# Kernel optimization log

Measured on AMD Instinct MI355X. Metric: run time of the kernel, lower is better.

## Reference

```python
import jax, jax.numpy as jnp
import numpy as np

DIM = 256
D_STATE = 16
D_INNER = 2 * DIM
D_CONV = 4
DT_RANK = (DIM + 15) // 16  # 'auto' = ceil(dim/16)
B_SZ, H, W = 8, 32, 32


def setup_inputs() -> dict:
    key = jax.random.key(0)
    ks = jax.random.split(key, 12)
    n = lambda k, s, sc=0.02: jax.random.normal(k, s, jnp.float32) * sc
    # Mamba1 dt init: dt ~ exp(U(log dt_min, log dt_max)), bias = inv_softplus(dt)
    dt = jnp.exp(jax.random.uniform(ks[5], (D_INNER,), jnp.float32,
                                    np.log(1e-3), np.log(1e-1)))
    return {
        "x": jax.random.normal(ks[0], (B_SZ, DIM, H, W), jnp.float32),
        "ln_g": jnp.ones((DIM,), jnp.float32),
        "ln_b": jnp.zeros((DIM,), jnp.float32),
        "in_proj_w": n(ks[1], (2 * D_INNER, DIM)),
        "conv_w": n(ks[2], (D_INNER, 1, D_CONV), 0.1),  # depthwise Conv1d kernel
        "conv_b": jnp.zeros((D_INNER,), jnp.float32),
        "x_proj_w": n(ks[3], (DT_RANK + 2 * D_STATE, D_INNER)),
        "dt_proj_w": n(ks[4], (D_INNER, DT_RANK), DT_RANK ** -0.5),
        "dt_proj_b": jnp.log(jnp.expm1(dt)),
        "A_log": jnp.log(jnp.broadcast_to(
            jnp.arange(1, D_STATE + 1, dtype=jnp.float32), (D_INNER, D_STATE))),
        "Dp": jnp.ones((D_INNER,), jnp.float32),
        "out_proj_w": n(ks[6], (DIM, D_INNER)),
        "mlp_ln_g": jnp.ones((DIM,), jnp.float32),
        "mlp_ln_b": jnp.zeros((DIM,), jnp.float32),
        "mlp_w1": n(ks[7], (4 * DIM, DIM)),
        "mlp_b1": jnp.zeros((4 * DIM,), jnp.float32),
        "mlp_w2": n(ks[8], (DIM, 4 * DIM)),
        "mlp_b2": jnp.zeros((DIM,), jnp.float32),
    }


def _layernorm(x, g, b):
    m = x.mean(-1, keepdims=True)
    v = x.var(-1, keepdims=True)
    return (x - m) * jax.lax.rsqrt(v + 1e-5) * g + b


def _selective_scan(u, dt, A, Bm, Cm, Dp):
    # u, dt: [B,L,Di]; Bm, Cm: [B,L,S]; A: [Di,S]; Dp: [Di]
    def step(h, t):
        dt_t, B_t, C_t, u_t = t  # [B,Di], [B,S], [B,S], [B,Di]
        dA = jnp.exp(dt_t[..., None] * A)                 # [B,Di,S]
        h = dA * h + dt_t[..., None] * B_t[:, None, :] * u_t[..., None]
        y = jnp.einsum('bds,bs->bd', h, C_t)
        return h, y

    h0 = jnp.zeros((u.shape[0], A.shape[0], A.shape[1]), u.dtype)
    xs = (dt.transpose(1, 0, 2), Bm.transpose(1, 0, 2),
          Cm.transpose(1, 0, 2), u.transpose(1, 0, 2))
    _, ys = jax.lax.scan(step, h0, xs)                    # ys: [L,B,Di]
    return ys.transpose(1, 0, 2) + u * Dp


def reference(x, ln_g, ln_b, in_proj_w, conv_w, conv_b, x_proj_w,
              dt_proj_w, dt_proj_b, A_log, Dp, out_proj_w,
              mlp_ln_g, mlp_ln_b, mlp_w1, mlp_b1, mlp_w2, mlp_b2):
    B, C, Hh, Ww = x.shape
    xf = x.reshape(B, C, Hh * Ww).transpose(0, 2, 1)      # [B,L,C]

    # ---- Mamba1 mixer with pre-LN residual ----
    xn = _layernorm(xf, ln_g, ln_b)
    xz = xn @ in_proj_w.T                                 # [B,L,2*Di]
    xi, z = jnp.split(xz, 2, axis=-1)
    # depthwise causal conv1d + SiLU
    xc = jax.lax.conv_general_dilated(
        xi.transpose(0, 2, 1), conv_w, (1,), [(D_CONV - 1, 0)],
        feature_group_count=D_INNER, dimension_numbers=('NCH', 'OIH', 'NCH'))
    xc = jax.nn.silu(xc + conv_b[None, :, None]).transpose(0, 2, 1)  # [B,L,Di]
    # input-dependent dt, B, C
    dbl = xc @ x_proj_w.T
    dt_r = dbl[..., :DT_RANK]
    Bm = dbl[..., DT_RANK:DT_RANK + D_STATE]
    Cm = dbl[..., DT_RANK + D_STATE:]
    dt = jax.nn.softplus(dt_r @ dt_proj_w.T + dt_proj_b)  # [B,L,Di]
    A = -jnp.exp(A_log)
    y = _selective_scan(xc, dt, A, Bm, Cm, Dp)
    y = y * jax.nn.silu(z)
    xf = xf + y @ out_proj_w.T

    # ---- gated MLP with pre-LN residual ----
    h = _layernorm(xf, mlp_ln_g, mlp_ln_b)
    h = jax.nn.gelu(h @ mlp_w1.T + mlp_b1, approximate=False) @ mlp_w2.T + mlp_b2
    xf = xf + h

    return xf.transpose(0, 2, 1).reshape(B, C, Hh, Ww)
```

## Files before the change

### kernel.cpp

```cpp
#include <hip/hip_runtime.h>
#include <math.h>

#define DIM      256
#define L_SEQ    1024
#define B_SZ     8
#define D_INNER  512
#define D_STATE  16
#define DT_RANK  16
#define N_TOK    (B_SZ * L_SEQ)
#define T_CH     64

typedef unsigned short u16;
typedef __attribute__((ext_vector_type(4))) float f32x4;
typedef __attribute__((ext_vector_type(8))) short short8;
struct __align__(8) us4 { u16 x, y, z, w; };

#define OFF_WB   0
#define OFF_XT   471040
#define OFF_XNB  2568192
#define OFF_XZ   3616768
#define OFF_XC   12005376
#define OFF_DBL  16199680
#define OFF_DT   16592896
#define OFF_YB   20787200
#define OFF_XF2  OFF_XC
#define OFF_TOUT (OFF_XC + 2097152)
#define OFF_H    OFF_XZ
#define WB_IN    0
#define WB_OUT   262144
#define WB_W1    393216
#define WB_W2    655360
#define WB_XP    917504

__device__ __forceinline__ u16 f2b(float f) {
    unsigned int u = __float_as_uint(f);
    return (u16)((u + 0x7fffu + ((u >> 16) & 1u)) >> 16);
}

__global__ __launch_bounds__(256) void cvt5_kernel(const float* __restrict__ a,
                                                   const float* __restrict__ b,
                                                   const float* __restrict__ c,
                                                   const float* __restrict__ d,
                                                   const float* __restrict__ e,
                                                   u16* __restrict__ out) {
    int i = blockIdx.x * 256 + threadIdx.x;
    const float* src; int off;
    if (i < 262144)      { src = a; off = i; }
    else if (i < 393216) { src = b; off = i - 262144; }
    else if (i < 655360) { src = c; off = i - 393216; }
    else if (i < 917504) { src = d; off = i - 655360; }
    else                 { src = e; off = i - 917504; }
    out[i] = f2b(src[off]);
}

__global__ __launch_bounds__(256) void tin_kernel(const float* __restrict__ x,
                                                  float* __restrict__ XT) {
    __shared__ float tile[64][65];
    int bb = blockIdx.x >> 6, c0 = ((blockIdx.x >> 4) & 3) << 6, l0 = (blockIdx.x & 15) << 6;
    int tr = threadIdx.x >> 6, tc = threadIdx.x & 63;
    const float* src = x + ((size_t)bb * 256 + c0) * 1024 + l0;
    #pragma unroll
    for (int i = 0; i < 16; i++) tile[tr + i * 4][tc] = src[(size_t)(tr + i * 4) * 1024 + tc];
    __syncthreads();
    float* dst = XT + ((size_t)bb * 1024 + l0) * 256 + c0;
    #pragma unroll
    for (int i = 0; i < 16; i++) dst[(size_t)(tr + i * 4) * 256 + tc] = tile[tc][tr + i * 4];
}

__global__ __launch_bounds__(256) void tout_kernel(const float* __restrict__ T,
                                                   float* __restrict__ outp) {
    __shared__ float tile[64][65];
    int bb = blockIdx.x >> 6, c0 = ((blockIdx.x >> 4) & 3) << 6, l0 = (blockIdx.x & 15) << 6;
    int tr = threadIdx.x >> 6, tc = threadIdx.x & 63;
    const float* src = T + ((size_t)bb * 1024 + l0) * 256 + c0;
    #pragma unroll
    for (int i = 0; i < 16; i++) tile[tr + i * 4][tc] = src[(size_t)(tr + i * 4) * 256 + tc];
    __syncthreads();
    float* dst = outp + ((size_t)bb * 256 + c0) * 1024 + l0;
    #pragma unroll
    for (int i = 0; i < 16; i++) dst[(size_t)(tr + i * 4) * 1024 + tc] = tile[tc][tr + i * 4];
}

__global__ __launch_bounds__(256) void ln_kernel(const float* __restrict__ in,
                                                 const float* __restrict__ g,
                                                 const float* __restrict__ b,
                                                 u16* __restrict__ out) {
    int token = blockIdx.x;
    int c = threadIdx.x;
    float v = in[(size_t)token * DIM + c];
    float s = v, s2 = v * v;
    #pragma unroll
    for (int o = 32; o; o >>= 1) {
        s  += __shfl_down(s, o);
        s2 += __shfl_down(s2, o);
    }
    __shared__ float red[8];
    int w = threadIdx.x >> 6;
    if ((threadIdx.x & 63) == 0) { red[w] = s; red[4 + w] = s2; }
    __syncthreads();
    if (threadIdx.x == 0) {
        float a = 0.f, aa = 0.f;
        for (int i = 0; i < 4; i++) { a += red[i]; aa += red[4 + i]; }
        red[0] = a; red[4] = aa;
    }
    __syncthreads();
    float mean = red[0] * (1.f / DIM);
    float var  = red[4] * (1.f / DIM) - mean * mean;
    float rstd = rsqrtf(var + 1e-5f);
    out[(size_t)token * DIM + c] = f2b((v - mean) * rstd * g[c] + b[c]);
}

__device__ __forceinline__ void gload16(const void* g, void* l) {
    __builtin_amdgcn_global_load_lds(
        (const __attribute__((address_space(1))) unsigned int*)g,
        (__attribute__((address_space(3))) unsigned int*)l,
        16, 0, 0);
}

template <int EPI>
__global__ __launch_bounds__(256) void gemm_mfma(const u16* __restrict__ A,
                                                 const u16* __restrict__ W,
                                                 void* __restrict__ Cout,
                                                 int M, int N, int K,
                                                 const float* __restrict__ bias,
                                                 const float* __restrict__ extra) {
    __shared__ u16 Als[4096];
    __shared__ u16 Bls[4096];
    int tid = threadIdx.x;
    int w = tid >> 6, l = tid & 63;
    int m0 = blockIdx.y << 7, n0 = blockIdx.x << 7;

    int srow = tid >> 2;
    int scol = (tid & 3) << 3;
    const u16* Ag  = A + (size_t)(m0 + srow) * K + scol;
    const u16* Ag2 = A + (size_t)(m0 + 64 + srow) * K + scol;
    const u16* Wg  = W + (size_t)(n0 + srow) * K + scol;
    const u16* Wg2 = W + (size_t)(n0 + 64 + srow) * K + scol;
    u16* Ab0 = Als + (w << 9);
    u16* Ab1 = Als + 2048 + (w << 9);
    u16* Bb0 = Bls + (w << 9);
    u16* Bb1 = Bls + 2048 + (w << 9);

    int wr = (w >> 1) << 6, wc = (w & 1) << 6;
    int fr = l & 15, fk = (l >> 4) << 3;

    f32x4 acc[4][4] = {};
    for (int k0 = 0; k0 < K; k0 += 32) {
        gload16(Ag + k0, Ab0);
        gload16(Ag2 + k0, Ab1);
        gload16(Wg + k0, Bb0);
        gload16(Wg2 + k0, Bb1);
        __syncthreads();
        short8 af[4], bfr[4];
        #pragma unroll
        for (int i = 0; i < 4; i++)
            af[i] = *(const short8*)&Als[(wr + i * 16 + fr) * 32 + fk];
        #pragma unroll
        for (int j = 0; j < 4; j++)
            bfr[j] = *(const short8*)&Bls[(wc + j * 16 + fr) * 32 + fk];
        #pragma unroll
        for (int i = 0; i < 4; i++)
            #pragma unroll
            for (int j = 0; j < 4; j++)
                acc[i][j] = __builtin_amdgcn_mfma_f32_16x16x32_bf16(af[i], bfr[j], acc[i][j], 0, 0, 0);
        __syncthreads();
    }

    int cr = (l >> 4) << 2;
    int ccol = l & 15;
    #pragma unroll
    for (int i = 0; i < 4; i++) {
        #pragma unroll
        for (int j = 0; j < 4; j++) {
            int n = n0 + wc + j * 16 + ccol;
            #pragma unroll
            for (int r = 0; r < 4; r++) {
                int m = m0 + wr + i * 16 + cr + r;
                float v = acc[i][j][r];
                if (EPI == 0) {
                    ((float*)Cout)[(size_t)m * N + n] = v;
                } else if (EPI == 1) {
                    ((float*)Cout)[(size_t)m * N + n] = v + extra[(size_t)m * DIM + n];
                } else if (EPI == 2) {
                    v += bias[n];
                    ((u16*)Cout)[(size_t)m * N + n] = f2b(0.5f * v * (1.f + erff(v * 0.70710678118f)));
                } else {
                    v += bias[n] + extra[(size_t)m * DIM + n];
                    ((float*)Cout)[(size_t)m * N + n] = v;
                }
            }
        }
    }
}

__global__ __launch_bounds__(256) void conv_kernel(const float* __restrict__ XZ,
                                                   const float* __restrict__ cw,
                                                   const float* __restrict__ cb,
                                                   float* __restrict__ XC) {
    int idx = blockIdx.x * 256 + threadIdx.x;
    int d = idx & 511;
    int token = idx >> 9;
    int l = token & 1023, b = token >> 10;
    const float* base = XZ + (size_t)b * L_SEQ * 1024 + d;
    float acc = cb[d];
    #pragma unroll
    for (int j = 0; j < 4; j++) {
        int ls = l - 3 + j;
        if (ls >= 0) acc = fmaf(base[(size_t)ls * 1024], cw[d * 4 + j], acc);
    }
    XC[(size_t)token * 512 + d] = acc / (1.f + __expf(-acc));
}

__global__ __launch_bounds__(128) void xproj3_kernel(const float* __restrict__ XCf,
                                                     const u16* __restrict__ WXP,
                                                     float* __restrict__ DBL) {
    __shared__ float dbl_s[32][49];
    int tid = threadIdx.x;
    int w = tid >> 6, l = tid & 63;
    int m0 = blockIdx.x << 5;
    int fr = l & 15, fk = (l >> 4) << 3;
    const float* Af = XCf + (size_t)(m0 + (w << 4) + fr) * 512 + fk;
    const u16* Wb = WXP + (size_t)fr * 512 + fk;
    f32x4 acc[3] = {};
    for (int k0 = 0; k0 < 512; k0 += 32) {
        float4 fa = *(const float4*)(Af + k0);
        float4 fb = *(const float4*)(Af + k0 + 4);
        short8 a0;
        a0[0] = (short)f2b(fa.x); a0[1] = (short)f2b(fa.y);
        a0[2] = (short)f2b(fa.z); a0[3] = (short)f2b(fa.w);
        a0[4] = (short)f2b(fb.x); a0[5] = (short)f2b(fb.y);
        a0[6] = (short)f2b(fb.z); a0[7] = (short)f2b(fb.w);
        short8 b0 = *(const short8*)(Wb + k0);
        short8 b1 = *(const short8*)(Wb + 16 * 512 + k0);
        short8 b2 = *(const short8*)(Wb + 32 * 512 + k0);
        acc[0] = __builtin_amdgcn_mfma_f32_16x16x32_bf16(a0, b0, acc[0], 0, 0, 0);
        acc[1] = __builtin_amdgcn_mfma_f32_16x16x32_bf16(a0, b1, acc[1], 0, 0, 0);
        acc[2] = __builtin_amdgcn_mfma_f32_16x16x32_bf16(a0, b2, acc[2], 0, 0, 0);
    }
    int cr = (l >> 4) << 2, ccol = l & 15;
    #pragma unroll
    for (int j = 0; j < 3; j++)
        #pragma unroll
        for (int r = 0; r < 4; r++)
            dbl_s[(w << 4) + cr + r][j * 16 + ccol] = acc[j][r];
    __syncthreads();
    #pragma unroll
    for (int it = 0; it < 3; it++) {
        int fidx = it * 512 + tid * 4;
        int row = fidx / 48, col = fidx % 48;
        float4 v;
        v.x = dbl_s[row][col]; v.y = dbl_s[row][col + 1];
        v.z = dbl_s[row][col + 2]; v.w = dbl_s[row][col + 3];
        *(float4*)(DBL + (size_t)(m0 + row) * 48 + col) = v;
    }
}

__global__ __launch_bounds__(256) void dtproj_kernel(const float* __restrict__ DBL,
                                                     const float* __restrict__ wdt,
                                                     const float* __restrict__ wdb,
                                                     float* __restrict__ DT) {
    int idx = blockIdx.x * 256 + threadIdx.x;
    int token = idx >> 7, q = idx & 127;
    int d0 = q << 2;
    const float4* dtr4 = (const float4*)(DBL + (size_t)token * 48);
    float4 t0 = dtr4[0], t1 = dtr4[1], t2 = dtr4[2], t3 = dtr4[3];
    float4 ov;
    #pragma unroll
    for (int qq = 0; qq < 4; qq++) {
        int d = d0 + qq;
        const float4* wr = (const float4*)(wdt + (size_t)d * 16);
        float4 w0 = wr[0], w1 = wr[1], w2 = wr[2], w3 = wr[3];
        float a = wdb[d];
        a += t0.x * w0.x + t0.y * w0.y + t0.z * w0.z + t0.w * w0.w;
        a += t1.x * w1.x + t1.y * w1.y + t1.z * w1.z + t1.w * w1.w;
        a += t2.x * w2.x + t2.y * w2.y + t2.z * w2.z + t2.w * w2.w;
        a += t3.x * w3.x + t3.y * w3.y + t3.z * w3.z + t3.w * w3.w;
        ((float*)&ov)[qq] = (a > 20.f) ? a : log1pf(__expf(a));
    }
    *(float4*)(DT + (size_t)token * 512 + d0) = ov;
}

__global__ __launch_bounds__(256) void scan_kernel(const float* __restrict__ U,
                                                   const float* __restrict__ DBL,
                                                   const float* __restrict__ DT,
                                                   const float* __restrict__ XZ,
                                                   const float* __restrict__ A_log,
                                                   const float* __restrict__ Dp,
                                                   u16* __restrict__ YB) {
    __shared__ float s_dt[2][T_CH][16];
    __shared__ float s_u [2][T_CH][16];
    __shared__ float s_BC[2][T_CH][32];
    __shared__ float s_z [2][T_CH][16];
    __shared__ float s_y [2][T_CH * 17];

    int blk = blockIdx.x;
    int b = blk >> 5, ch = blk & 31;
    int tid = threadIdx.x;
    int s = tid & 15, dl = tid >> 4;
    int d = ch * 16 + dl;
    int w = tid >> 6;

    float Ads = -__expf(A_log[d * D_STATE + s]);
    float Dv = Dp[d];

    const float* DTb = DT  + (size_t)b * L_SEQ * D_INNER + ch * 16;
    const float* Ub  = U   + (size_t)b * L_SEQ * D_INNER + ch * 16;
    const float* DBb = DBL + (size_t)b * L_SEQ * 48 + 16;
    const float* Zb  = XZ  + (size_t)b * L_SEQ * 1024 + 512 + ch * 16;
    u16* Yb          = YB  + (size_t)b * L_SEQ * D_INNER + ch * 16;

    int r16 = tid >> 2, q16 = (tid & 3) << 2;
    int r32 = tid >> 3, q32 = (tid & 7) << 2;

    #define STAGE(c, bf) { \
        int t0_ = (c) * T_CH; \
        gload16(DTb + (size_t)(t0_ + r16) * 512 + q16, &s_dt[bf][0][0] + (w << 8)); \
        gload16(Ub  + (size_t)(t0_ + r16) * 512 + q16, &s_u [bf][0][0] + (w << 8)); \
        gload16(Zb  + (size_t)(t0_ + r16) * 1024 + q16, &s_z[bf][0][0] + (w << 8)); \
        gload16(DBb + (size_t)(t0_ + r32) * 48 + q32, &s_BC[bf][0][0] + (w << 8)); \
        gload16(DBb + (size_t)(t0_ + 32 + r32) * 48 + q32, &s_BC[bf][0][0] + 1024 + (w << 8)); \
    }

    float h = 0.f;
    int bf = 0;
    STAGE(0, 0);
    __syncthreads();

    for (int c = 0; c < L_SEQ / T_CH; c++) {
        if (c + 1 < L_SEQ / T_CH) STAGE(c + 1, bf ^ 1);
        int yb = c & 1;
        #pragma unroll 1
        for (int tb = 0; tb < 4; tb++) {
            float da[16], db[16], cc[16], pr[16];
            float myud = 0.f;
            #pragma unroll
            for (int j = 0; j < 16; j++) {
                int t = (tb << 4) + j;
                float dtv = s_dt[bf][t][dl];
                float uv  = s_u [bf][t][dl];
                float bs  = s_BC[bf][t][s];
                float cs  = s_BC[bf][t][16 + s];
                da[j] = __expf(dtv * Ads);
                db[j] = dtv * bs * uv;
                cc[j] = cs;
                myud = (s == j) ? uv * Dv : myud;
            }
            #pragma unroll
            for (int j = 0; j < 16; j++) {
                h = fmaf(da[j], h, db[j]);
                pr[j] = h * cc[j];
            }
            float w8[8];
            #pragma unroll
            for (int k = 0; k < 8; k++) {
                float a = pr[2 * k], bv = pr[2 * k + 1];
                float keep = (s & 1) ? bv : a;
                float send = (s & 1) ? a : bv;
                w8[k] = keep + __shfl_xor(send, 1);
            }
            float u4[4];
            #pragma unroll
            for (int k = 0; k < 4; k++) {
                float a = w8[2 * k], bv = w8[2 * k + 1];
                float keep = (s & 2) ? bv : a;
                float send = (s & 2) ? a : bv;
                u4[k] = keep + __shfl_xor(send, 2);
            }
            float x2[2];
            #pragma unroll
            for (int k = 0; k < 2; k++) {
                float a = u4[2 * k], bv = u4[2 * k + 1];
                float keep = (s & 4) ? bv : a;
                float send = (s & 4) ? a : bv;
                x2[k] = keep + __shfl_xor(send, 4);
            }
            float a0 = x2[0], b0 = x2[1];
            float keep = (s & 8) ? b0 : a0;
            float send = (s & 8) ? a0 : b0;
            float res = keep + __shfl_xor(send, 8);
            int t = (tb << 4) + s;
            float zv = s_z[bf][t][dl];
            float y = res + myud;
            s_y[yb][t * 17 + dl] = y * (zv / (1.f + __expf(-zv)));
        }
        __syncthreads();
        {
            int t0_ = c * T_CH;
            int tt = tid >> 2, qq = (tid & 3) << 2;
            us4 o;
            o.x = f2b(s_y[yb][tt * 17 + qq + 0]);
            o.y = f2b(s_y[yb][tt * 17 + qq + 1]);
            o.z = f2b(s_y[yb][tt * 17 + qq + 2]);
            o.w = f2b(s_y[yb][tt * 17 + qq + 3]);
            *(us4*)(Yb + (size_t)(t0_ + tt) * 512 + qq) = o;
        }
        bf ^= 1;
    }
    #undef STAGE
}

extern "C" void kernel_launch(void* const* d_in, const int* in_sizes, int n_in,
                              void* d_out, int out_size, void* d_ws, size_t ws_size,
                              hipStream_t stream) {
    (void)in_sizes; (void)n_in; (void)out_size; (void)ws_size;
    const float* x         = (const float*)d_in[0];
    const float* ln_g      = (const float*)d_in[1];
    const float* ln_b      = (const float*)d_in[2];
    const float* in_proj_w = (const float*)d_in[3];
    const float* conv_w    = (const float*)d_in[4];
    const float* conv_b    = (const float*)d_in[5];
    const float* x_proj_w  = (const float*)d_in[6];
    const float* dt_proj_w = (const float*)d_in[7];
    const float* dt_proj_b = (const float*)d_in[8];
    const float* A_log     = (const float*)d_in[9];
    const float* Dp        = (const float*)d_in[10];
    const float* out_proj_w= (const float*)d_in[11];
    const float* mlp_ln_g  = (const float*)d_in[12];
    const float* mlp_ln_b  = (const float*)d_in[13];
    const float* mlp_w1    = (const float*)d_in[14];
    const float* mlp_b1    = (const float*)d_in[15];
    const float* mlp_w2    = (const float*)d_in[16];
    const float* mlp_b2    = (const float*)d_in[17];

    float* ws  = (float*)d_ws;
    u16*   WB  = (u16*)(ws + OFF_WB);
    float* XT  = ws + OFF_XT;
    u16*   XNB = (u16*)(ws + OFF_XNB);
    float* XZ  = ws + OFF_XZ;
    float* XC  = ws + OFF_XC;
    float* DBL = ws + OFF_DBL;
    float* DT  = ws + OFF_DT;
    u16*   YB  = (u16*)(ws + OFF_YB);
    float* XF2 = ws + OFF_XF2;
    float* TOUT= ws + OFF_TOUT;
    u16*   H   = (u16*)(ws + OFF_H);
    float* out = (float*)d_out;

    cvt5_kernel<<<3680, 256, 0, stream>>>(in_proj_w, out_proj_w, mlp_w1, mlp_w2, x_proj_w, WB);
    tin_kernel<<<512, 256, 0, stream>>>(x, XT);
    ln_kernel<<<N_TOK, 256, 0, stream>>>(XT, ln_g, ln_b, XNB);
    gemm_mfma<0><<<dim3(8, 64), 256, 0, stream>>>(XNB, WB + WB_IN, XZ, N_TOK, 1024, 256, nullptr, nullptr);
    conv_kernel<<<(N_TOK * D_INNER) / 256, 256, 0, stream>>>(XZ, conv_w, conv_b, XC);
    xproj3_kernel<<<256, 128, 0, stream>>>(XC, WB + WB_XP, DBL);
    dtproj_kernel<<<4096, 256, 0, stream>>>(DBL, dt_proj_w, dt_proj_b, DT);
    scan_kernel<<<256, 256, 0, stream>>>(XC, DBL, DT, XZ, A_log, Dp, YB);
    gemm_mfma<1><<<dim3(2, 64), 256, 0, stream>>>(YB, WB + WB_OUT, XF2, N_TOK, 256, 512, nullptr, XT);
    ln_kernel<<<N_TOK, 256, 0, stream>>>(XF2, mlp_ln_g, mlp_ln_b, XNB);
    gemm_mfma<2><<<dim3(8, 64), 256, 0, stream>>>(XNB, WB + WB_W1, H, N_TOK, 1024, 256, mlp_b1, nullptr);
    gemm_mfma<3><<<dim3(2, 64), 256, 0, stream>>>(H, WB + WB_W2, TOUT, N_TOK, 256, 1024, mlp_b2, XF2);
    tout_kernel<<<512, 256, 0, stream>>>(TOUT, out);
}
```

Baseline: 324.3 us.

## Split selective scan into chunked partial scans with carry combine and fixup

Splits the sequential selective scan over 1024 tokens into four 256-token chunks, scanned in parallel from zero state, which raises the grid from 256 to 1024 blocks. A small combine kernel propagates the chunk-end states using the cumulative dt decay, and a fixup kernel adds the carried-in state's contribution, the D skip term and the SiLU gate for chunks 1-3. The aim is to fill more of the GPU's compute units during the scan. The cost is two extra launches, a second pass that rereads dt/C/u/z and the partial y, and intermediate y rounded to bf16 before the correction is added.

```diff
diff --git a/kernel.cpp b/kernel.cpp
--- a/kernel.cpp
+++ b/kernel.cpp
@@ -9,6 +9,7 @@
 #define DT_RANK  16
 #define N_TOK    (B_SZ * L_SEQ)
 #define T_CH     64
+#define CL       256
 
 typedef unsigned short u16;
 typedef __attribute__((ext_vector_type(4))) float f32x4;
@@ -23,6 +24,9 @@
 #define OFF_DBL  16199680
 #define OFF_DT   16592896
 #define OFF_YB   20787200
+#define OFF_HE   22884352
+#define OFF_HI   23146496
+#define OFF_CD   23408640
 #define OFF_XF2  OFF_XC
 #define OFF_TOUT (OFF_XC + 2097152)
 #define OFF_H    OFF_XZ
@@ -35,6 +39,9 @@
 __device__ __forceinline__ u16 f2b(float f) {
     unsigned int u = __float_as_uint(f);
     return (u16)((u + 0x7fffu + ((u >> 16) & 1u)) >> 16);
+}
+__device__ __forceinline__ float b2f(u16 v) {
+    return __uint_as_float(((unsigned)v) << 16);
 }
 
 __global__ __launch_bounds__(256) void cvt5_kernel(const float* __restrict__ a,
@@ -280,13 +287,15 @@
     *(float4*)(DT + (size_t)token * 512 + d0) = ov;
 }
 
-__global__ __launch_bounds__(256) void scan_kernel(const float* __restrict__ U,
-                                                   const float* __restrict__ DBL,
-                                                   const float* __restrict__ DT,
-                                                   const float* __restrict__ XZ,
-                                                   const float* __restrict__ A_log,
-                                                   const float* __restrict__ Dp,
-                                                   u16* __restrict__ YB) {
+__global__ __launch_bounds__(256) void scan_part(const float* __restrict__ U,
+                                                 const float* __restrict__ DBL,
+                                                 const float* __restrict__ DT,
+                                                 const float* __restrict__ XZ,
+                                                 const float* __restrict__ A_log,
+                                                 const float* __restrict__ Dp,
+                                                 u16* __restrict__ YB,
+                                                 float* __restrict__ HEND,
+                                                 float* __restrict__ CUMDT) {
     __shared__ float s_dt[2][T_CH][16];
     __shared__ float s_u [2][T_CH][16];
     __shared__ float s_BC[2][T_CH][32];
@@ -294,7 +303,7 @@
     __shared__ float s_y [2][T_CH * 17];
 
     int blk = blockIdx.x;
-    int b = blk >> 5, ch = blk & 31;
+    int c = blk & 3, ch = (blk >> 2) & 31, b = blk >> 7;
     int tid = threadIdx.x;
     int s = tid & 15, dl = tid >> 4;
     int d = ch * 16 + dl;
@@ -312,8 +321,8 @@
     int r16 = tid >> 2, q16 = (tid & 3) << 2;
     int r32 = tid >> 3, q32 = (tid & 7) << 2;
 
-    #define STAGE(c, bf) { \
-        int t0_ = (c) * T_CH; \
+    #define STAGE(t0a, bf) { \
+        int t0_ = (t0a); \
         gload16(DTb + (size_t)(t0_ + r16) * 512 + q16, &s_dt[bf][0][0] + (w << 8)); \
         gload16(Ub  + (size_t)(t0_ + r16) * 512 + q16, &s_u [bf][0][0] + (w << 8)); \
         gload16(Zb  + (size_t)(t0_ + r16) * 1024 + q16, &s_z[bf][0][0] + (w << 8)); \
@@ -321,17 +330,17 @@
         gload16(DBb + (size_t)(t0_ + 32 + r32) * 48 + q32, &s_BC[bf][0][0] + 1024 + (w << 8)); \
     }
 
-    float h = 0.f;
+    float h = 0.f, cumdt = 0.f;
     int bf = 0;
-    STAGE(0, 0);
+    STAGE(c * CL, 0);
     __syncthreads();
 
-    for (int c = 0; c < L_SEQ / T_CH; c++) {
-        if (c + 1 < L_SEQ / T_CH) STAGE(c + 1, bf ^ 1);
-        int yb = c & 1;
+    for (int cc = 0; cc < CL / T_CH; cc++) {
+        if (cc + 1 < CL / T_CH) STAGE(c * CL + (cc + 1) * T_CH, bf ^ 1);
+        int yb = cc & 1;
         #pragma unroll 1
         for (int tb = 0; tb < 4; tb++) {
-            float da[16], db[16], cc[16], pr[16];
+            float da[16], db[16], cv[16], pr[16];
             float myud = 0.f;
             #pragma unroll
             for (int j = 0; j < 16; j++) {
@@ -340,15 +349,16 @@
                 float uv  = s_u [bf][t][dl];
                 float bs  = s_BC[bf][t][s];
                 float cs  = s_BC[bf][t][16 + s];
+                cumdt += dtv;
                 da[j] = __expf(dtv * Ads);
                 db[j] = dtv * bs * uv;
-                cc[j] = cs;
+                cv[j] = cs;
                 myud = (s == j) ? uv * Dv : myud;
             }
             #pragma unroll
             for (int j = 0; j < 16; j++) {
                 h = fmaf(da[j], h, db[j]);
-                pr[j] = h * cc[j];
+                pr[j] = h * cv[j];
             }
             float w8[8];
             #pragma unroll
@@ -379,13 +389,18 @@
             float send = (s & 8) ? a0 : b0;
             float res = keep + __shfl_xor(send, 8);
             int t = (tb << 4) + s;
-            float zv = s_z[bf][t][dl];
-            float y = res + myud;
-            s_y[yb][t * 17 + dl] = y * (zv / (1.f + __expf(-zv)));
+            float y;
+            if (c == 0) {
+                float zv = s_z[bf][t][dl];
+                y = (res + myud) * (zv / (1.f + __expf(-zv)));
+            } else {
+                y = res;
+            }
+            s_y[yb][t * 17 + dl] = y;
         }
         __syncthreads();
         {
-            int t0_ = c * T_CH;
+            int t0_ = c * CL + cc * T_CH;
             int tt = tid >> 2, qq = (tid & 3) << 2;
             us4 o;
             o.x = f2b(s_y[yb][tt * 17 + qq + 0]);
@@ -397,6 +412,143 @@
         bf ^= 1;
     }
     #undef STAGE
+    HEND[(((size_t)b * 4 + c) * 512 + d) * 16 + s] = h;
+    if (s == 0) CUMDT[((size_t)b * 4 + c) * 512 + d] = cumdt;
+}
+
+__global__ __launch_bounds__(256) void scan_comb(const float* __restrict__ A_log,
+                                                 const float* __restrict__ HEND,
+                                                 const float* __restrict__ CUMDT,
+                                                 float* __restrict__ HINIT) {
+    int idx = blockIdx.x * 256 + threadIdx.x;
+    int s = idx & 15, d = (idx >> 4) & 511, b = idx >> 13;
+    float As = -__expf(A_log[d * D_STATE + s]);
+    float hi = HEND[(((size_t)b * 4 + 0) * 512 + d) * 16 + s];
+    HINIT[(((size_t)b * 4 + 1) * 512 + d) * 16 + s] = hi;
+    #pragma unroll
+    for (int c = 2; c < 4; c++) {
+        float cd = CUMDT[((size_t)b * 4 + (c - 1)) * 512 + d];
+        float he = HEND[(((size_t)b * 4 + (c - 1)) * 512 + d) * 16 + s];
+        hi = he + __expf(As * cd) * hi;
+        HINIT[(((size_t)b * 4 + c) * 512 + d) * 16 + s] = hi;
+    }
+}
+
+__global__ __launch_bounds__(256) void scan_fix(const float* __restrict__ U,
+                                                const float* __restrict__ DBL,
+                                                const float* __restrict__ DT,
+                                                const float* __restrict__ XZ,
+                                                const float* __restrict__ A_log,
+                                                const float* __restrict__ Dp,
+                                                const float* __restrict__ HINIT,
+                                                u16* __restrict__ YB) {
+    __shared__ float s_dt[2][T_CH][16];
+    __shared__ float s_C [2][T_CH][16];
+    __shared__ float s_u [2][T_CH][16];
+    __shared__ float s_z [2][T_CH][16];
+    __shared__ u16   s_yr[2][T_CH][16];
+    __shared__ float s_y [2][T_CH * 17];
+
+    int blk = blockIdx.x;
+    int c = (blk % 3) + 1;
+    int t3 = blk / 3;
+    int ch = t3 & 31, b = t3 >> 5;
+    int tid = threadIdx.x;
+    int s = tid & 15, dl = tid >> 4;
+    int d = ch * 16 + dl;
+    int w = tid >> 6;
+
+    float Ads = -__expf(A_log[d * D_STATE + s]);
+    float Dv = Dp[d];
+    float h0 = HINIT[(((size_t)b * 4 + c) * 512 + d) * 16 + s];
+
+    const float* DTb = DT  + (size_t)b * L_SEQ * D_INNER + ch * 16;
+    const float* Cb  = DBL + (size_t)b * L_SEQ * 48 + 32;
+    const float* Ub  = U   + (size_t)b * L_SEQ * D_INNER + ch * 16;
+    const float* Zb  = XZ  + (size_t)b * L_SEQ * 1024 + 512 + ch * 16;
+    u16* Yb          = YB  + (size_t)b * L_SEQ * D_INNER + ch * 16;
+
+    int r16 = tid >> 2, q16 = (tid & 3) << 2;
+    int ry = (tid & 127) >> 1, qy = (tid & 1) << 3;
+
+    #define STAGEF(t0a, bf) { \
+        int t0_ = (t0a); \
+        gload16(DTb + (size_t)(t0_ + r16) * 512 + q16, &s_dt[bf][0][0] + (w << 8)); \
+        gload16(Cb  + (size_t)(t0_ + r16) * 48 + q16, &s_C[bf][0][0] + (w << 8)); \
+        gload16(Ub  + (size_t)(t0_ + r16) * 512 + q16, &s_u[bf][0][0] + (w << 8)); \
+        gload16(Zb  + (size_t)(t0_ + r16) * 1024 + q16, &s_z[bf][0][0] + (w << 8)); \
+        if (tid < 128) gload16(Yb + (size_t)(t0_ + ry) * 512 + qy, &s_yr[bf][0][0] + (w << 9)); \
+    }
+
+    float cumdt = 0.f;
+    int bf = 0;
+    STAGEF(c * CL, 0);
+    __syncthreads();
+
+    for (int cc = 0; cc < CL / T_CH; cc++) {
+        if (cc + 1 < CL / T_CH) STAGEF(c * CL + (cc + 1) * T_CH, bf ^ 1);
+        int yb = cc & 1;
+        #pragma unroll 1
+        for (int tb = 0; tb < 4; tb++) {
+            float pr[16];
+            float myud = 0.f;
+            #pragma unroll
+            for (int j = 0; j < 16; j++) {
+                int t = (tb << 4) + j;
+                float dtv = s_dt[bf][t][dl];
+                cumdt += dtv;
+                float cs = s_C[bf][t][s];
+                pr[j] = __expf(Ads * cumdt) * cs * h0;
+                myud = (s == j) ? s_u[bf][t][dl] * Dv : myud;
+            }
+            float w8[8];
+            #pragma unroll
+            for (int k = 0; k < 8; k++) {
+                float a = pr[2 * k], bv = pr[2 * k + 1];
+                float keep = (s & 1) ? bv : a;
+                float send = (s & 1) ? a : bv;
+                w8[k] = keep + __shfl_xor(send, 1);
+            }
+            float u4[4];
+            #pragma unroll
+            for (int k = 0; k < 4; k++) {
+                float a = w8[2 * k], bv = w8[2 * k + 1];
+                float keep = (s & 2) ? bv : a;
+                float send = (s & 2) ? a : bv;
+                u4[k] = keep + __shfl_xor(send, 2);
+            }
+            float x2[2];
+            #pragma unroll
+            for (int k = 0; k < 2; k++) {
+                float a = u4[2 * k], bv = u4[2 * k + 1];
+                float keep = (s & 4) ? bv : a;
+                float send = (s & 4) ? a : bv;
+                x2[k] = keep + __shfl_xor(send, 4);
+            }
+            float a0 = x2[0], b0 = x2[1];
+            float keep = (s & 8) ? b0 : a0;
+            float send = (s & 8) ? a0 : b0;
+            float res = keep + __shfl_xor(send, 8);
+            int t = (tb << 4) + s;
+            float yrv = b2f(s_yr[bf][t][dl]);
+            float zv = s_z[bf][t][dl];
+            float y = yrv + res + myud;
+            s_y[yb][t * 17 + dl] = y * (zv / (1.f + __expf(-zv)));
+        }
+        __syncthreads();
+        {
+            int t0_ = c * CL + cc * T_CH;
+            int tt = tid >> 2, qq = (tid & 3) << 2;
+            us4 o;
+            o.x = f2b(s_y[yb][tt * 17 + qq + 0]);
+            o.y = f2b(s_y[yb][tt * 17 + qq + 1]);
+            o.z = f2b(s_y[yb][tt * 17 + qq + 2]);
+            o.w = f2b(s_y[yb][tt * 17 + qq + 3]);
+            *(us4*)(Yb + (size_t)(t0_ + tt) * 512 + qq) = o;
+        }
+        bf ^= 1;
+    }
+    #undef STAGEF
 }
 
 extern "C" void kernel_launch(void* const* d_in, const int* in_sizes, int n_in,
@@ -431,6 +583,9 @@
     float* DBL = ws + OFF_DBL;
     float* DT  = ws + OFF_DT;
     u16*   YB  = (u16*)(ws + OFF_YB);
+    float* HE  = ws + OFF_HE;
+    float* HI  = ws + OFF_HI;
+    float* CD  = ws + OFF_CD;
     float* XF2 = ws + OFF_XF2;
     float* TOUT= ws + OFF_TOUT;
     u16*   H   = (u16*)(ws + OFF_H);
@@ -443,7 +598,9 @@
     conv_kernel<<<(N_TOK * D_INNER) / 256, 256, 0, stream>>>(XZ, conv_w, conv_b, XC);
     xproj3_kernel<<<256, 128, 0, stream>>>(XC, WB + WB_XP, DBL);
     dtproj_kernel<<<4096, 256, 0, stream>>>(DBL, dt_proj_w, dt_proj_b, DT);
-    scan_kernel<<<256, 256, 0, stream>>>(XC, DBL, DT, XZ, A_log, Dp, YB);
+    scan_part<<<1024, 256, 0, stream>>>(XC, DBL, DT, XZ, A_log, Dp, YB, HE, CD);
+    scan_comb<<<256, 256, 0, stream>>>(A_log, HE, CD, HI);
+    scan_fix<<<768, 256, 0, stream>>>(XC, DBL, DT, XZ, A_log, Dp, HI, YB);
     gemm_mfma<1><<<dim3(2, 64), 256, 0, stream>>>(YB, WB + WB_OUT, XF2, N_TOK, 256, 512, nullptr, XT);
     ln_kernel<<<N_TOK, 256, 0, stream>>>(XF2, mlp_ln_g, mlp_ln_b, XNB);
     gemm_mfma<2><<<dim3(8, 64), 256, 0, stream>>>(XNB, WB + WB_W1, H, N_TOK, 1024, 256, mlp_b1, nullptr);
```

After: 339.2 us. +4.6%, slower.

## Store XZ and XC intermediates as bf16 across conv, xproj and scan

Applied to the files above, without the earlier changes.

The in_proj GEMM gains a bf16 epilogue, so the XZ buffer is written in bf16. The conv kernel now reads bf16, handles four channels per thread, and writes XC in bf16. xproj then loads bf16 operands directly without converting, and the scan stages u and z in bf16 shared memory. The aim is to halve memory traffic for these large intermediates, at the cost of extra rounding on u, z and the conv inputs.

```diff
diff --git a/kernel.cpp b/kernel.cpp
--- a/kernel.cpp
+++ b/kernel.cpp
@@ -36,6 +36,9 @@
     unsigned int u = __float_as_uint(f);
     return (u16)((u + 0x7fffu + ((u >> 16) & 1u)) >> 16);
 }
+__device__ __forceinline__ float b2f(u16 v) {
+    return __uint_as_float(((unsigned)v) << 16);
+}
 
 __global__ __launch_bounds__(256) void cvt5_kernel(const float* __restrict__ a,
                                                    const float* __restrict__ b,
@@ -184,34 +187,48 @@
                 } else if (EPI == 2) {
                     v += bias[n];
                     ((u16*)Cout)[(size_t)m * N + n] = f2b(0.5f * v * (1.f + erff(v * 0.70710678118f)));
-                } else {
+                } else if (EPI == 3) {
                     v += bias[n] + extra[(size_t)m * DIM + n];
                     ((float*)Cout)[(size_t)m * N + n] = v;
+                } else {
+                    ((u16*)Cout)[(size_t)m * N + n] = f2b(v);
                 }
             }
         }
     }
 }
 
-__global__ __launch_bounds__(256) void conv_kernel(const float* __restrict__ XZ,
+__global__ __launch_bounds__(256) void conv_kernel(const u16* __restrict__ XZB,
                                                    const float* __restrict__ cw,
                                                    const float* __restrict__ cb,
-                                                   float* __restrict__ XC) {
+                                                   u16* __restrict__ XCB) {
     int idx = blockIdx.x * 256 + threadIdx.x;
-    int d = idx & 511;
-    int token = idx >> 9;
+    int d4 = (idx & 127) << 2;
+    int token = idx >> 7;
     int l = token & 1023, b = token >> 10;
-    const float* base = XZ + (size_t)b * L_SEQ * 1024 + d;
-    float acc = cb[d];
+    const u16* base = XZB + (size_t)b * L_SEQ * 1024 + d4;
+    float4 bias4 = *(const float4*)(cb + d4);
+    float acc0 = bias4.x, acc1 = bias4.y, acc2 = bias4.z, acc3 = bias4.w;
     #pragma unroll
     for (int j = 0; j < 4; j++) {
         int ls = l - 3 + j;
-        if (ls >= 0) acc = fmaf(base[(size_t)ls * 1024], cw[d * 4 + j], acc);
-    }
-    XC[(size_t)token * 512 + d] = acc / (1.f + __expf(-acc));
-}
-
-__global__ __launch_bounds__(128) void xproj3_kernel(const float* __restrict__ XCf,
+        if (ls >= 0) {
+            us4 xv = *(const us4*)(base + (size_t)ls * 1024);
+            acc0 = fmaf(b2f(xv.x), cw[(d4 + 0) * 4 + j], acc0);
+            acc1 = fmaf(b2f(xv.y), cw[(d4 + 1) * 4 + j], acc1);
+            acc2 = fmaf(b2f(xv.z), cw[(d4 + 2) * 4 + j], acc2);
+            acc3 = fmaf(b2f(xv.w), cw[(d4 + 3) * 4 + j], acc3);
+        }
+    }
+    us4 o;
+    o.x = f2b(acc0 / (1.f + __expf(-acc0)));
+    o.y = f2b(acc1 / (1.f + __expf(-acc1)));
+    o.z = f2b(acc2 / (1.f + __expf(-acc2)));
+    o.w = f2b(acc3 / (1.f + __expf(-acc3)));
+    *(us4*)(XCB + (size_t)token * 512 + d4) = o;
+}
+
+__global__ __launch_bounds__(128) void xproj3_kernel(const u16* __restrict__ XCB,
                                                      const u16* __restrict__ WXP,
                                                      float* __restrict__ DBL) {
     __shared__ float dbl_s[32][49];
@@ -219,17 +236,11 @@
     int w = tid >> 6, l = tid & 63;
     int m0 = blockIdx.x << 5;
     int fr = l & 15, fk = (l >> 4) << 3;
-    const float* Af = XCf + (size_t)(m0 + (w << 4) + fr) * 512 + fk;
+    const u16* Ab = XCB + (size_t)(m0 + (w << 4) + fr) * 512 + fk;
     const u16* Wb = WXP + (size_t)fr * 512 + fk;
     f32x4 acc[3] = {};
     for (int k0 = 0; k0 < 512; k0 += 32) {
-        float4 fa = *(const float4*)(Af + k0);
-        float4 fb = *(const float4*)(Af + k0 + 4);
-        short8 a0;
-        a0[0] = (short)f2b(fa.x); a0[1] = (short)f2b(fa.y);
-        a0[2] = (short)f2b(fa.z); a0[3] = (short)f2b(fa.w);
-        a0[4] = (short)f2b(fb.x); a0[5] = (short)f2b(fb.y);
-        a0[6] = (short)f2b(fb.z); a0[7] = (short)f2b(fb.w);
+        short8 a0 = *(const short8*)(Ab + k0);
         short8 b0 = *(const short8*)(Wb + k0);
         short8 b1 = *(const short8*)(Wb + 16 * 512 + k0);
         short8 b2 = *(const short8*)(Wb + 32 * 512 + k0);
@@ -280,17 +291,17 @@
     *(float4*)(DT + (size_t)token * 512 + d0) = ov;
 }
 
-__global__ __launch_bounds__(256) void scan_kernel(const float* __restrict__ U,
+__global__ __launch_bounds__(256) void scan_kernel(const u16* __restrict__ U,
                                                    const float* __restrict__ DBL,
                                                    const float* __restrict__ DT,
-                                                   const float* __restrict__ XZ,
+                                                   const u16* __restrict__ XZB,
                                                    const float* __restrict__ A_log,
                                                    const float* __restrict__ Dp,
                                                    u16* __restrict__ YB) {
     __shared__ float s_dt[2][T_CH][16];
-    __shared__ float s_u [2][T_CH][16];
+    __shared__ u16   s_u [2][T_CH][16];
     __shared__ float s_BC[2][T_CH][32];
-    __shared__ float s_z [2][T_CH][16];
+    __shared__ u16   s_z [2][T_CH][16];
     __shared__ float s_y [2][T_CH * 17];
 
     int blk = blockIdx.x;
@@ -304,21 +315,25 @@
     float Dv = Dp[d];
 
     const float* DTb = DT  + (size_t)b * L_SEQ * D_INNER + ch * 16;
-    const float* Ub  = U   + (size_t)b * L_SEQ * D_INNER + ch * 16;
+    const u16*   Ub  = U   + (size_t)b * L_SEQ * D_INNER + ch * 16;
     const float* DBb = DBL + (size_t)b * L_SEQ * 48 + 16;
-    const float* Zb  = XZ  + (size_t)b * L_SEQ * 1024 + 512 + ch * 16;
+    const u16*   Zb  = XZB + (size_t)b * L_SEQ * 1024 + 512 + ch * 16;
     u16* Yb          = YB  + (size_t)b * L_SEQ * D_INNER + ch * 16;
 
     int r16 = tid >> 2, q16 = (tid & 3) << 2;
     int r32 = tid >> 3, q32 = (tid & 7) << 2;
+    int rhb = (tid & 127) >> 1, qhb = (tid & 1) << 3;
 
     #define STAGE(c, bf) { \
         int t0_ = (c) * T_CH; \
         gload16(DTb + (size_t)(t0_ + r16) * 512 + q16, &s_dt[bf][0][0] + (w << 8)); \
-        gload16(Ub  + (size_t)(t0_ + r16) * 512 + q16, &s_u [bf][0][0] + (w << 8)); \
-        gload16(Zb  + (size_t)(t0_ + r16) * 1024 + q16, &s_z[bf][0][0] + (w << 8)); \
         gload16(DBb + (size_t)(t0_ + r32) * 48 + q32, &s_BC[bf][0][0] + (w << 8)); \
         gload16(DBb + (size_t)(t0_ + 32 + r32) * 48 + q32, &s_BC[bf][0][0] + 1024 + (w << 8)); \
+        if (tid < 128) { \
+            gload16(Ub + (size_t)(t0_ + rhb) * 512 + qhb, (u16*)&s_u[bf][0][0] + ((w & 1) << 9)); \
+        } else { \
+            gload16(Zb + (size_t)(t0_ + rhb) * 1024 + qhb, (u16*)&s_z[bf][0][0] + ((w & 1) << 9)); \
+        } \
     }
 
     float h = 0.f;
@@ -337,7 +352,7 @@
             for (int j = 0; j < 16; j++) {
                 int t = (tb << 4) + j;
                 float dtv = s_dt[bf][t][dl];
-                float uv  = s_u [bf][t][dl];
+                float uv  = b2f(s_u[bf][t][dl]);
                 float bs  = s_BC[bf][t][s];
                 float cs  = s_BC[bf][t][16 + s];
                 da[j] = __expf(dtv * Ads);
@@ -379,7 +394,7 @@
             float send = (s & 8) ? a0 : b0;
             float res = keep + __shfl_xor(send, 8);
             int t = (tb << 4) + s;
-            float zv = s_z[bf][t][dl];
+            float zv = b2f(s_z[bf][t][dl]);
             float y = res + myud;
             s_y[yb][t * 17 + dl] = y * (zv / (1.f + __expf(-zv)));
         }
@@ -426,8 +441,8 @@
     u16*   WB  = (u16*)(ws + OFF_WB);
     float* XT  = ws + OFF_XT;
     u16*   XNB = (u16*)(ws + OFF_XNB);
-    float* XZ  = ws + OFF_XZ;
-    float* XC  = ws + OFF_XC;
+    u16*   XZB = (u16*)(ws + OFF_XZ);
+    u16*   XCB = (u16*)(ws + OFF_XC);
     float* DBL = ws + OFF_DBL;
     float* DT  = ws + OFF_DT;
     u16*   YB  = (u16*)(ws + OFF_YB);
@@ -439,11 +454,11 @@
     cvt5_kernel<<<3680, 256, 0, stream>>>(in_proj_w, out_proj_w, mlp_w1, mlp_w2, x_proj_w, WB);
     tin_kernel<<<512, 256, 0, stream>>>(x, XT);
     ln_kernel<<<N_TOK, 256, 0, stream>>>(XT, ln_g, ln_b, XNB);
-    gemm_mfma<0><<<dim3(8, 64), 256, 0, stream>>>(XNB, WB + WB_IN, XZ, N_TOK, 1024, 256, nullptr, nullptr);
-    conv_kernel<<<(N_TOK * D_INNER) / 256, 256, 0, stream>>>(XZ, conv_w, conv_b, XC);
-    xproj3_kernel<<<256, 128, 0, stream>>>(XC, WB + WB_XP, DBL);
+    gemm_mfma<4><<<dim3(8, 64), 256, 0, stream>>>(XNB, WB + WB_IN, XZB, N_TOK, 1024, 256, nullptr, nullptr);
+    conv_kernel<<<4096, 256, 0, stream>>>(XZB, conv_w, conv_b, XCB);
+    xproj3_kernel<<<256, 128, 0, stream>>>(XCB, WB + WB_XP, DBL);
     dtproj_kernel<<<4096, 256, 0, stream>>>(DBL, dt_proj_w, dt_proj_b, DT);
-    scan_kernel<<<256, 256, 0, stream>>>(XC, DBL, DT, XZ, A_log, Dp, YB);
+    scan_kernel<<<256, 256, 0, stream>>>(XCB, DBL, DT, XZB, A_log, Dp, YB);
     gemm_mfma<1><<<dim3(2, 64), 256, 0, stream>>>(YB, WB + WB_OUT, XF2, N_TOK, 256, 512, nullptr, XT);
     ln_kernel<<<N_TOK, 256, 0, stream>>>(XF2, mlp_ln_g, mlp_ln_b, XNB);
     gemm_mfma<2><<<dim3(8, 64), 256, 0, stream>>>(XNB, WB + WB_W1, H, N_TOK, 1024, 256, mlp_b1, nullptr);
```

New measurement: 329.0 us. No clear change (+1.5%).
